# Performance work log

Hardware: AMD Instinct MI355X
Metric: run time of the kernel (lower is better)

Reference implementation:

```python
import jax, jax.numpy as jnp
import numpy as np

NUM_OPS, B, T, D = 8, 8, 512, 1024


def setup_inputs() -> dict:
    key = jax.random.key(0)
    k1, k2, k3, k4 = jax.random.split(key, 4)
    x = jax.random.normal(k1, (B, T, D), dtype=jnp.float32)
    W = jax.random.normal(k2, (NUM_OPS, D, D), dtype=jnp.float32) * 0.02
    b = jnp.zeros((NUM_OPS, D), dtype=jnp.float32)
    logits = 0.001 * jax.random.normal(k3, (NUM_OPS,), dtype=jnp.float32)
    # uniform noise for Gumbel sampling (matches tf.random.uniform in sample_without_replacement)
    u = jax.random.uniform(k4, (NUM_OPS,), dtype=jnp.float32, minval=1e-6, maxval=1.0 - 1e-6)
    return {"x": x, "W": W, "b": b, "logits": logits, "u": u}


def reference(x, W, b, logits, u):
    # weights = softmax(logits); gumbel top-1 over log(weights) == log_softmax(logits)
    gumbel = -jnp.log(-jnp.log(u))
    idx = jnp.argmax(jax.nn.log_softmax(logits) + gumbel)
    # forward of ops_times_mask_binary: sum over ON ops (num_on_samples=1 -> single op)
    out = jnp.einsum('btd,de->bte', x, W[idx]) + b[idx]  # [B,T,D]
    return out
```

## Files before the change

### kernel.cpp

```cpp
#include <hip/hip_runtime.h>

typedef unsigned short u16;
typedef unsigned int u32;
typedef __attribute__((ext_vector_type(8))) short bf16x8;
typedef __attribute__((ext_vector_type(4))) float f32x4;

#define NUM_OPS 8
#define M_DIM 4096
#define K_DIM 1024
#define N_DIM 1024
#define BK 32
#define PITCH 40
#define KITERS (K_DIM / BK)


__device__ __forceinline__ int compute_idx(const float* __restrict__ logits,
                                           const float* __restrict__ u) {
  int best = 0; float bv = -3.4e38f;
#pragma unroll
  for (int i = 0; i < NUM_OPS; ++i) {
    float g = -logf(-logf(u[i]));
    float v = logits[i] + g;
    if (v > bv) { bv = v; best = i; }
  }
  return best;
}

__device__ __forceinline__ u32 pk2(float a, float b) {
  u32 ua = __float_as_uint(a) + 0x8000u;
  u32 ub = __float_as_uint(b) + 0x8000u;
  return (ua >> 16) | (ub & 0xffff0000u);
}

__global__ __launch_bounds__(512) void fused_kernel(
    const float* __restrict__ x, const float* __restrict__ W,
    const float* __restrict__ bvec, const float* __restrict__ logits,
    const float* __restrict__ u, float* __restrict__ out) {
  __shared__ u16 sA[2][128 * PITCH];
  __shared__ u16 sB[2][128 * PITCH];

  const int tid = threadIdx.x;
  const int w = tid >> 6, L = tid & 63;
  const int m0 = blockIdx.y * 128;
  const int n0 = blockIdx.x * 128;

  const int idx = compute_idx(logits, u);
  const float* Wi = W + (size_t)idx * K_DIM * N_DIM;

  const int am = tid >> 2, akq = tid & 3;
  const float* gA = x + (size_t)(m0 + am) * K_DIM + akq * 8;
  const int lA = am * PITCH + akq * 8;

  const int bn = tid & 127, bkg = tid >> 7;
  const float* gB = Wi + (size_t)(bkg * 8) * N_DIM + n0 + bn;
  const int lB = bn * PITCH + bkg * 8;

  const int wm = w & 1, wn = w >> 1;
  int aoff[4], boff[2];
#pragma unroll
  for (int mt = 0; mt < 4; ++mt)
    aoff[mt] = (64 * wm + 16 * mt + (L & 15)) * PITCH + (L >> 4) * 8;
#pragma unroll
  for (int nt = 0; nt < 2; ++nt)
    boff[nt] = (32 * wn + 16 * nt + (L & 15)) * PITCH + (L >> 4) * 8;

  f32x4 acc[4][2] = {};

  float4 ra0 = *(const float4*)(gA);
  float4 ra1 = *(const float4*)(gA + 4);
  float rb[8];
#pragma unroll
  for (int j = 0; j < 8; ++j) rb[j] = gB[(size_t)j * N_DIM];

  for (int kk = 0; kk < KITERS; ++kk) {
    const int cur = kk & 1;
    uint4 pa; pa.x = pk2(ra0.x, ra0.y); pa.y = pk2(ra0.z, ra0.w);
    pa.z = pk2(ra1.x, ra1.y); pa.w = pk2(ra1.z, ra1.w);
    *(uint4*)(&sA[cur][lA]) = pa;
    uint4 pb; pb.x = pk2(rb[0], rb[1]); pb.y = pk2(rb[2], rb[3]);
    pb.z = pk2(rb[4], rb[5]); pb.w = pk2(rb[6], rb[7]);
    *(uint4*)(&sB[cur][lB]) = pb;
    __syncthreads();

    if (kk + 1 < KITERS) {
      const float* gA2 = gA + (kk + 1) * BK;
      ra0 = *(const float4*)(gA2);
      ra1 = *(const float4*)(gA2 + 4);
      const float* gB2 = gB + (size_t)(kk + 1) * BK * N_DIM;
#pragma unroll
      for (int j = 0; j < 8; ++j) rb[j] = gB2[(size_t)j * N_DIM];
    }

    bf16x8 af[4], bf[2];
#pragma unroll
    for (int mt = 0; mt < 4; ++mt) af[mt] = *(const bf16x8*)(&sA[cur][aoff[mt]]);
#pragma unroll
    for (int nt = 0; nt < 2; ++nt) bf[nt] = *(const bf16x8*)(&sB[cur][boff[nt]]);
#pragma unroll
    for (int mt = 0; mt < 4; ++mt)
#pragma unroll
      for (int nt = 0; nt < 2; ++nt)
        acc[mt][nt] = __builtin_amdgcn_mfma_f32_16x16x32_bf16(
            af[mt], bf[nt], acc[mt][nt], 0, 0, 0);
  }

  const float* bi = bvec + (size_t)idx * N_DIM;
#pragma unroll
  for (int mt = 0; mt < 4; ++mt) {
    int row = m0 + 64 * wm + 16 * mt + (L >> 4) * 4;
#pragma unroll
    for (int nt = 0; nt < 2; ++nt) {
      int col = n0 + 32 * wn + 16 * nt + (L & 15);
      float bv = bi[col];
#pragma unroll
      for (int r = 0; r < 4; ++r)
        out[(size_t)(row + r) * N_DIM + col] = acc[mt][nt][r] + bv;
    }
  }
}


extern "C" void kernel_launch(void* const* d_in, const int* in_sizes, int n_in,
                              void* d_out, int out_size, void* d_ws, size_t ws_size,
                              hipStream_t stream) {
  const float* x      = (const float*)d_in[0];
  const float* W      = (const float*)d_in[1];
  const float* bvec   = (const float*)d_in[2];
  const float* logits = (const float*)d_in[3];
  const float* u      = (const float*)d_in[4];
  float* out = (float*)d_out;

  dim3 grid(N_DIM / 128, M_DIM / 128);
  fused_kernel<<<grid, 512, 0, stream>>>(x, W, bvec, logits, u, out);
}
```

Before: 120.0 us.

## Pre-transpose selected weight to bf16 workspace and stream it via global_load_lds

```diff
diff --git a/kernel.cpp b/kernel.cpp
--- a/kernel.cpp
+++ b/kernel.cpp
@@ -10,20 +10,14 @@
 #define K_DIM 1024
 #define N_DIM 1024
 #define BK 32
+#define KITERS (K_DIM / BK)
 #define PITCH 40
-#define KITERS (K_DIM / BK)
 
 
-__device__ __forceinline__ int compute_idx(const float* __restrict__ logits,
-                                           const float* __restrict__ u) {
-  int best = 0; float bv = -3.4e38f;
-#pragma unroll
-  for (int i = 0; i < NUM_OPS; ++i) {
-    float g = -logf(-logf(u[i]));
-    float v = logits[i] + g;
-    if (v > bv) { bv = v; best = i; }
-  }
-  return best;
+__device__ __forceinline__ u16 f2b(float f) {
+  union { float f; u32 u; } v; v.f = f;
+  u32 r = v.u + 0x7fffu + ((v.u >> 16) & 1u);
+  return (u16)(r >> 16);
 }
 
 __device__ __forceinline__ u32 pk2(float a, float b) {
@@ -32,63 +26,106 @@
   return (ua >> 16) | (ub & 0xffff0000u);
 }
 
-__global__ __launch_bounds__(512) void fused_kernel(
-    const float* __restrict__ x, const float* __restrict__ W,
+__device__ __forceinline__ int compute_idx(const float* __restrict__ logits,
+                                           const float* __restrict__ u) {
+  int best = 0; float bv = -3.4e38f;
+#pragma unroll
+  for (int i = 0; i < NUM_OPS; ++i) {
+    float v = logits[i] - logf(-logf(u[i]));
+    if (v > bv) { bv = v; best = i; }
+  }
+  return best;
+}
+
+__device__ __forceinline__ void gld_lds16(const void* g, void* l) {
+  __builtin_amdgcn_global_load_lds(
+      (__attribute__((address_space(1))) void*)(g),
+      (__attribute__((address_space(3))) void*)(unsigned)(unsigned long long)(l),
+      16, 0, 0);
+}
+
+__global__ void prep_kernel(const float* __restrict__ W,
+                            const float* __restrict__ logits,
+                            const float* __restrict__ u,
+                            u16* __restrict__ wt) {
+  __shared__ u16 t[64][66];
+  const int tid = threadIdx.x, wb = blockIdx.x;
+  const int kt = wb >> 4, nt = wb & 15;
+  const int idx = compute_idx(logits, u);
+  const float* Wi = W + (size_t)idx * K_DIM * N_DIM;
+#pragma unroll
+  for (int it = 0; it < 16; ++it) {
+    int i = it * 256 + tid;
+    int r = i >> 6, c = i & 63;
+    t[r][c] = f2b(Wi[(size_t)(kt * 64 + r) * N_DIM + nt * 64 + c]);
+  }
+  __syncthreads();
+#pragma unroll
+  for (int it = 0; it < 8; ++it) {
+    int i = it * 256 + tid;
+    int n = i >> 5, kp = i & 31;
+    u32 lo = t[2 * kp][n], hi = t[2 * kp + 1][n];
+    *(u32*)(wt + (size_t)(nt * 64 + n) * K_DIM + kt * 64 + 2 * kp) =
+        lo | (hi << 16);
+  }
+}
+
+__global__ __launch_bounds__(256) void gemm_kernel(
+    const float* __restrict__ x, const u16* __restrict__ wt,
     const float* __restrict__ bvec, const float* __restrict__ logits,
     const float* __restrict__ u, float* __restrict__ out) {
   __shared__ u16 sA[2][128 * PITCH];
-  __shared__ u16 sB[2][128 * PITCH];
+  __shared__ u16 sB[2][64 * 32];
 
   const int tid = threadIdx.x;
   const int w = tid >> 6, L = tid & 63;
   const int m0 = blockIdx.y * 128;
-  const int n0 = blockIdx.x * 128;
+  const int n0 = blockIdx.x * 64;
 
-  const int idx = compute_idx(logits, u);
-  const float* Wi = W + (size_t)idx * K_DIM * N_DIM;
+  const int arow = tid >> 1, akh = tid & 1;
+  const float* gA = x + (size_t)(m0 + arow) * K_DIM + akh * 16;
+  const int lA = arow * PITCH + akh * 16;
 
-  const int am = tid >> 2, akq = tid & 3;
-  const float* gA = x + (size_t)(m0 + am) * K_DIM + akq * 8;
-  const int lA = am * PITCH + akq * 8;
-
-  const int bn = tid & 127, bkg = tid >> 7;
-  const float* gB = Wi + (size_t)(bkg * 8) * N_DIM + n0 + bn;
-  const int lB = bn * PITCH + bkg * 8;
+  const int brow = 16 * w + (L >> 2);
+  const int kqs = (L & 3) ^ (((L >> 2) & 3) ^ (L >> 4));
+  const u16* gB = wt + (size_t)(n0 + brow) * K_DIM + kqs * 8;
+  const int lB = w * 512 + L * 8;
 
   const int wm = w & 1, wn = w >> 1;
+  const int swf = (L & 3) ^ ((L >> 2) & 3);
   int aoff[4], boff[2];
 #pragma unroll
   for (int mt = 0; mt < 4; ++mt)
     aoff[mt] = (64 * wm + 16 * mt + (L & 15)) * PITCH + (L >> 4) * 8;
 #pragma unroll
   for (int nt = 0; nt < 2; ++nt)
-    boff[nt] = (32 * wn + 16 * nt + (L & 15)) * PITCH + (L >> 4) * 8;
+    boff[nt] = (32 * wn + 16 * nt + (L & 15)) * 32 + ((L >> 4) ^ swf) * 8;
 
   f32x4 acc[4][2] = {};
 
-  float4 ra0 = *(const float4*)(gA);
-  float4 ra1 = *(const float4*)(gA + 4);
-  float rb[8];
+  gld_lds16(gB, &sB[0][lB]);
+  float4 ra[4];
 #pragma unroll
-  for (int j = 0; j < 8; ++j) rb[j] = gB[(size_t)j * N_DIM];
+  for (int i = 0; i < 4; ++i) ra[i] = *(const float4*)(gA + i * 4);
 
   for (int kk = 0; kk < KITERS; ++kk) {
-    const int cur = kk & 1;
-    uint4 pa; pa.x = pk2(ra0.x, ra0.y); pa.y = pk2(ra0.z, ra0.w);
-    pa.z = pk2(ra1.x, ra1.y); pa.w = pk2(ra1.z, ra1.w);
-    *(uint4*)(&sA[cur][lA]) = pa;
-    uint4 pb; pb.x = pk2(rb[0], rb[1]); pb.y = pk2(rb[2], rb[3]);
-    pb.z = pk2(rb[4], rb[5]); pb.w = pk2(rb[6], rb[7]);
-    *(uint4*)(&sB[cur][lB]) = pb;
+    const int cur = kk & 1, nxt = cur ^ 1;
+
+    uint4 p0, p1;
+    p0.x = pk2(ra[0].x, ra[0].y); p0.y = pk2(ra[0].z, ra[0].w);
+    p0.z = pk2(ra[1].x, ra[1].y); p0.w = pk2(ra[1].z, ra[1].w);
+    p1.x = pk2(ra[2].x, ra[2].y); p1.y = pk2(ra[2].z, ra[2].w);
+    p1.z = pk2(ra[3].x, ra[3].y); p1.w = pk2(ra[3].z, ra[3].w);
+    *(uint4*)(&sA[cur][lA]) = p0;
+    *(uint4*)(&sA[cur][lA + 8]) = p1;
+
     __syncthreads();
 
     if (kk + 1 < KITERS) {
+      gld_lds16(gB + (kk + 1) * BK, &sB[nxt][lB]);
       const float* gA2 = gA + (kk + 1) * BK;
-      ra0 = *(const float4*)(gA2);
-      ra1 = *(const float4*)(gA2 + 4);
-      const float* gB2 = gB + (size_t)(kk + 1) * BK * N_DIM;
 #pragma unroll
-      for (int j = 0; j < 8; ++j) rb[j] = gB2[(size_t)j * N_DIM];
+      for (int i = 0; i < 4; ++i) ra[i] = *(const float4*)(gA2 + i * 4);
     }
 
     bf16x8 af[4], bf[2];
@@ -104,6 +141,7 @@
             af[mt], bf[nt], acc[mt][nt], 0, 0, 0);
   }
 
+  const int idx = compute_idx(logits, u);
   const float* bi = bvec + (size_t)idx * N_DIM;
 #pragma unroll
   for (int mt = 0; mt < 4; ++mt) {
@@ -130,6 +168,9 @@
   const float* u      = (const float*)d_in[4];
   float* out = (float*)d_out;
 
-  dim3 grid(N_DIM / 128, M_DIM / 128);
-  fused_kernel<<<grid, 512, 0, stream>>>(x, W, bvec, logits, u, out);
+  u16* wt = (u16*)d_ws;
+
+  prep_kernel<<<256, 256, 0, stream>>>(W, logits, u, wt);
+  dim3 grid(N_DIM / 64, M_DIM / 128);
+  gemm_kernel<<<grid, 256, 0, stream>>>(x, wt, bvec, logits, u, out);
 }
```

New measurement: 120.8 us. No clear change (+0.7%).
